# Kernel optimization log

Hardware: AMD Instinct MI355X
Metric: run time of the kernel (lower is better)

Reference implementation:

```python
import jax, jax.numpy as jnp
import numpy as np
from jax import lax


def setup_inputs() -> dict:
    key = jax.random.key(0)
    k1, k2 = jax.random.split(key)
    B, T, C, U, W = 8, 4096, 512, 512, 2
    inputs = jax.random.normal(k1, (B, T, C), dtype=jnp.float32)
    kernel = jax.random.normal(k2, (W, C, 3 * U), dtype=jnp.float32) * (1.0 / np.sqrt(W * C))
    bias = jnp.zeros((3 * U,), dtype=jnp.float32)
    return {"inputs": inputs, "kernel": kernel, "bias": bias}


def _fo_pool(x, f):
    # x, f: [B, T, U]; c_t = f_t * c_{t-1} + (1 - f_t) * x_t, c_0 = 0
    xT = jnp.swapaxes(x, 0, 1)  # [T, B, U]
    fT = jnp.swapaxes(f, 0, 1)
    c0 = jnp.zeros(x.shape[:1] + x.shape[2:], dtype=x.dtype)  # [B, U]

    def step(c, fx):
        ft, xt = fx
        c = ft * c + (1.0 - ft) * xt
        return c, c

    _, cT = lax.scan(step, c0, (fT, xT))
    return jnp.swapaxes(cT, 0, 1)  # [B, T, U]


def reference(inputs, kernel, bias):
    # Conv1D, padding='same', stride=1, NWC layout
    gates = lax.conv_general_dilated(
        inputs, kernel, window_strides=(1,), padding='SAME',
        dimension_numbers=('NWC', 'WIO', 'NWC')) + bias  # [B, T, 3U]
    x, forget, output = jnp.split(gates, 3, axis=-1)
    x = jnp.tanh(x)
    forget = jax.nn.sigmoid(forget)
    c = _fo_pool(x, forget)
    h = jax.nn.sigmoid(output) * c
    return h
```

## Files before the change

### kernel.cpp

```cpp
#include <hip/hip_runtime.h>

typedef unsigned short u16;
typedef unsigned int u32;
typedef _Float16 f16;
typedef __attribute__((ext_vector_type(8))) _Float16 half8;
typedef __attribute__((ext_vector_type(2))) __fp16 fp16x2;
typedef __attribute__((ext_vector_type(4))) float float4_;
typedef __attribute__((ext_vector_type(4))) unsigned short ushort4_;
typedef __attribute__((ext_vector_type(4))) unsigned int u32x4;

union hu { f16 h; u16 u; };

__device__ __forceinline__ u32 pkrtz(float a, float b) {
    fp16x2 t = __builtin_amdgcn_cvt_pkrtz(a, b);
    union { fp16x2 h; u32 u; } cv; cv.h = t;
    return cv.u;
}

__device__ __forceinline__ void gl16(const u16* g, u16* l) {
    __builtin_amdgcn_global_load_lds(
        (const __attribute__((address_space(1))) void*)g,
        (__attribute__((address_space(3))) void*)l, 16, 0, 0);
}

#define Bsz 8
#define Tsz 4096
#define Csz 512
#define Usz 512
#define NG  1536
#define KK  1024
#define MM  32768
#define NCH 64
#define CHL 64

__global__ void prep_a(const float* __restrict__ in, u16* __restrict__ A16) {
    int gid = blockIdx.x * 256 + threadIdx.x;
    int idx8 = gid * 8;
    int c8 = idx8 & 511;
    int row = idx8 >> 9;
    int b = (u32)row / 4097u;
    int t = row - b * 4097;
    u32x4 w;
    if (t == Tsz) {
        w = (u32x4)0;
    } else {
        const float* p = in + ((size_t)(b * Tsz + t) << 9) + c8;
        float4_ v0 = *(const float4_*)p;
        float4_ v1 = *(const float4_*)(p + 4);
        w.x = pkrtz(v0.x, v0.y); w.y = pkrtz(v0.z, v0.w);
        w.z = pkrtz(v1.x, v1.y); w.w = pkrtz(v1.z, v1.w);
    }
    *(u32x4*)(A16 + idx8) = w;
}

__global__ void prep_k(const float* __restrict__ kern, u16* __restrict__ KT) {
    int n = blockIdx.x * 256 + threadIdx.x;
    int k = blockIdx.y;
    float v = kern[(size_t)k * NG + n];
    hu cv; cv.h = (f16)v;
    KT[(size_t)n * KK + k] = cv.u;
}

__global__ __launch_bounds__(256, 4) void gemm_gates(
    const u16* __restrict__ A16, const u16* __restrict__ KT,
    const float* __restrict__ bias,
    u16* __restrict__ X, u16* __restrict__ F, float* __restrict__ O)
{
    __shared__ u16 lA[8192], lB[8192];

    const int tid  = threadIdx.x;
    const int lane = tid & 63;
    const int wave = tid >> 6;

    const int g   = blockIdx.x;
    const int grp = g / 192;
    const int r   = g - grp * 192;
    const int nb  = r % 12;
    const int mb  = grp * 16 + r / 12;
    const int m0 = mb * 128;
    const int n0 = nb * 128;
    const int b  = m0 >> 12;
    const int t0 = m0 & 4095;
    const int arow0 = b * (Tsz + 1) + t0;

    float4_ acc[4][4];
    #pragma unroll
    for (int i = 0; i < 4; ++i)
        #pragma unroll
        for (int j = 0; j < 4; ++j) acc[i][j] = (float4_)0.0f;

    const int wm = (wave >> 1) * 64;
    const int wn = (wave & 1) * 64;
    const int ar = wm + (lane & 15);
    const int br = wn + (lane & 15);
    const int q  = lane >> 4;
    const int swz = lane & 7;

    for (int kc = 0; kc < KK; kc += 64) {
        __syncthreads();
        const int tap = kc >> 9;
        const int kin = kc & 511;
        const int ab = arow0 + tap;
        #pragma unroll
        for (int it = 0; it < 4; ++it) {
            const int s = it * 256 + tid;
            const int row = s >> 3, p = s & 7;
            const int c = p ^ (row & 7);
            gl16(A16 + (((size_t)(ab + row)) << 9) + kin + c * 8, lA + (s - lane) * 8);
        }
        #pragma unroll
        for (int it = 0; it < 4; ++it) {
            const int s = it * 256 + tid;
            const int row = s >> 3, p = s & 7;
            const int c = p ^ (row & 7);
            gl16(KT + (((size_t)(n0 + row)) << 10) + kc + c * 8, lB + (s - lane) * 8);
        }
        __syncthreads();

        #pragma unroll
        for (int s2 = 0; s2 < 2; ++s2) {
            half8 fa[4], fb[4];
            const int cc = (s2 * 4 + q) ^ swz;
            #pragma unroll
            for (int i = 0; i < 4; ++i) {
                fa[i] = *(const half8*)(lA + (ar + i * 16) * 64 + cc * 8);
                fb[i] = *(const half8*)(lB + (br + i * 16) * 64 + cc * 8);
            }
            #pragma unroll
            for (int mi = 0; mi < 4; ++mi)
                #pragma unroll
                for (int ni = 0; ni < 4; ++ni)
                    acc[mi][ni] = __builtin_amdgcn_mfma_f32_16x16x32_f16(fa[mi], fb[ni], acc[mi][ni], 0, 0, 0);
        }
    }

    const int plane = nb >> 2;
    const int rq = q * 4;
    const int cl = lane & 15;
    #pragma unroll
    for (int mi = 0; mi < 4; ++mi)
        #pragma unroll
        for (int ni = 0; ni < 4; ++ni) {
            const int gm = m0 + wm + mi * 16 + rq;
            const int gn = n0 + wn + ni * 16 + cl;
            const float bv = bias[gn];
            const int cp = gn & 511;
            #pragma unroll
            for (int r2 = 0; r2 < 4; ++r2) {
                float v = acc[mi][ni][r2] + bv;
                if (plane == 0) {
                    float res = 1.0f - 2.0f / (__expf(2.0f * v) + 1.0f);
                    hu cv; cv.h = (f16)res;
                    X[(size_t)(gm + r2) * Usz + cp] = cv.u;
                } else if (plane == 1) {
                    float res = 1.0f / (1.0f + __expf(-v));
                    hu cv; cv.h = (f16)res;
                    F[(size_t)(gm + r2) * Usz + cp] = cv.u;
                } else {
                    float res = 1.0f / (1.0f + __expf(-v));
                    O[(size_t)(gm + r2) * Usz + cp] = res;
                }
            }
        }
}

__device__ __forceinline__ float4_ x4(const u16* p) {
    ushort4_ xr = *(const ushort4_*)p;
    float4_ xv;
    #pragma unroll
    for (int j = 0; j < 4; ++j) { hu cv; cv.u = xr[j]; xv[j] = (float)cv.h; }
    return xv;
}

__global__ void scan_chunk(const u16* __restrict__ F, const u16* __restrict__ X,
                           float* __restrict__ CA, float* __restrict__ CB) {
    int g = blockIdx.x * 256 + threadIdx.x;
    int u4 = (g & 127) * 4;
    int bc = g >> 7;
    size_t base = (size_t)bc * CHL * Usz + u4;
    float4_ c = (float4_)0.0f, A = (float4_)1.0f;
    for (int i = 0; i < CHL; ++i) {
        float4_ fv = x4(F + base + (size_t)i * Usz);
        float4_ xv = x4(X + base + (size_t)i * Usz);
        c = fv * c + (1.0f - fv) * xv;
        A = A * fv;
    }
    *(float4_*)(CA + (size_t)bc * Usz + u4) = A;
    *(float4_*)(CB + (size_t)bc * Usz + u4) = c;
}

__global__ void scan_prefix(const float* __restrict__ CA, const float* __restrict__ CB,
                            float* __restrict__ CS) {
    int g = blockIdx.x * 256 + threadIdx.x;
    int u = g & 511;
    int b = g >> 9;
    float c = 0.0f;
    #pragma unroll 16
    for (int ch = 0; ch < NCH; ++ch) {
        int idx = (b * NCH + ch) * Usz + u;
        CS[idx] = c;
        c = CA[idx] * c + CB[idx];
    }
}

__global__ void scan_final(const u16* __restrict__ F, const u16* __restrict__ X,
                           const float* __restrict__ CS, float* __restrict__ out) {
    int g = blockIdx.x * 256 + threadIdx.x;
    int u4 = (g & 127) * 4;
    int bc = g >> 7;
    size_t base = (size_t)bc * CHL * Usz + u4;
    float4_ c = *(const float4_*)(CS + (size_t)bc * Usz + u4);
    for (int i = 0; i < CHL; ++i) {
        float4_ fv = x4(F + base + (size_t)i * Usz);
        float4_ xv = x4(X + base + (size_t)i * Usz);
        c = fv * c + (1.0f - fv) * xv;
        float4_ ov = *(const float4_*)(out + base + (size_t)i * Usz);
        *(float4_*)(out + base + (size_t)i * Usz) = ov * c;
    }
}

extern "C" void kernel_launch(void* const* d_in, const int* in_sizes, int n_in,
                              void* d_out, int out_size, void* d_ws, size_t ws_size,
                              hipStream_t stream) {
    const float* in   = (const float*)d_in[0];
    const float* kern = (const float*)d_in[1];
    const float* bias = (const float*)d_in[2];
    float* out = (float*)d_out;
    char* ws = (char*)d_ws;

    const size_t A16_B  = (size_t)Bsz * (Tsz + 1) * Csz * 2;
    const size_t OFF_KT = A16_B;
    const size_t OFF_F  = OFF_KT + (size_t)NG * KK * 2;
    const size_t OFF_X  = OFF_F + (size_t)MM * Usz * 2;
    const size_t OFF_CA = OFF_X + (size_t)MM * Usz * 2;
    const size_t CH_B   = (size_t)Bsz * NCH * Usz * 4;
    const size_t NEED   = OFF_CA + 3 * CH_B;

    if (ws_size < NEED) return;

    u16*   A16 = (u16*)ws;
    u16*   KT  = (u16*)(ws + OFF_KT);
    u16*   Fh  = (u16*)(ws + OFF_F);
    u16*   Xb  = (u16*)(ws + OFF_X);
    float* CA  = (float*)(ws + OFF_CA);
    float* CB  = CA + CH_B / 4;
    float* CS  = CB + CH_B / 4;

    prep_a<<<(int)(A16_B / 16 / 256), 256, 0, stream>>>(in, A16);
    prep_k<<<dim3(NG / 256, KK), 256, 0, stream>>>(kern, KT);
    gemm_gates<<<(MM / 128) * (NG / 128), 256, 0, stream>>>(A16, KT, bias, Xb, Fh, out);
    scan_chunk<<<Bsz * NCH * Usz / 4 / 256, 256, 0, stream>>>(Fh, Xb, CA, CB);
    scan_prefix<<<Bsz * Usz / 256, 256, 0, stream>>>(CA, CB, CS);
    scan_final<<<Bsz * NCH * Usz / 4 / 256, 256, 0, stream>>>(Fh, Xb, CS, out);
}
```

Measured before the change: 323.1 us.

## Merge prep kernels, store output gate as fp16, retile GEMM block order

Folds the two input-conversion kernels into one launch to remove a launch boundary. When the workspace is large enough, the sigmoid output gate is stored as fp16 in scratch instead of fp32 in the output buffer, which halves that gate's write and read traffic in the GEMM epilogue and final scan. The GEMM block-to-tile mapping changes to groups of 8 M-tiles across all 12 N-tiles, and the per-iteration address computation is hoisted out of the K loop. The fp16 output gate adds rounding error, and the fast path depends on the workspace size the harness supplies.

```diff
diff --git a/kernel.cpp b/kernel.cpp
--- a/kernel.cpp
+++ b/kernel.cpp
@@ -33,38 +33,44 @@
 #define NCH 64
 #define CHL 64
 
-__global__ void prep_a(const float* __restrict__ in, u16* __restrict__ A16) {
-    int gid = blockIdx.x * 256 + threadIdx.x;
-    int idx8 = gid * 8;
-    int c8 = idx8 & 511;
-    int row = idx8 >> 9;
-    int b = (u32)row / 4097u;
-    int t = row - b * 4097;
-    u32x4 w;
-    if (t == Tsz) {
-        w = (u32x4)0;
+#define PA_BLKS 8194
+#define PK_BLKS 6144
+
+__global__ void prep(const float* __restrict__ in, u16* __restrict__ A16,
+                     const float* __restrict__ kern, u16* __restrict__ KT) {
+    if (blockIdx.x < PA_BLKS) {
+        int gid = blockIdx.x * 256 + threadIdx.x;
+        int idx8 = gid * 8;
+        int c8 = idx8 & 511;
+        int row = idx8 >> 9;
+        int b = (u32)row / 4097u;
+        int t = row - b * 4097;
+        u32x4 w;
+        if (t == Tsz) {
+            w = (u32x4)0;
+        } else {
+            const float* p = in + ((size_t)(b * Tsz + t) << 9) + c8;
+            float4_ v0 = *(const float4_*)p;
+            float4_ v1 = *(const float4_*)(p + 4);
+            w.x = pkrtz(v0.x, v0.y); w.y = pkrtz(v0.z, v0.w);
+            w.z = pkrtz(v1.x, v1.y); w.w = pkrtz(v1.z, v1.w);
+        }
+        *(u32x4*)(A16 + idx8) = w;
     } else {
-        const float* p = in + ((size_t)(b * Tsz + t) << 9) + c8;
-        float4_ v0 = *(const float4_*)p;
-        float4_ v1 = *(const float4_*)(p + 4);
-        w.x = pkrtz(v0.x, v0.y); w.y = pkrtz(v0.z, v0.w);
-        w.z = pkrtz(v1.x, v1.y); w.w = pkrtz(v1.z, v1.w);
-    }
-    *(u32x4*)(A16 + idx8) = w;
-}
-
-__global__ void prep_k(const float* __restrict__ kern, u16* __restrict__ KT) {
-    int n = blockIdx.x * 256 + threadIdx.x;
-    int k = blockIdx.y;
-    float v = kern[(size_t)k * NG + n];
-    hu cv; cv.h = (f16)v;
-    KT[(size_t)n * KK + k] = cv.u;
+        int bk = blockIdx.x - PA_BLKS;
+        int k = bk / 6;
+        int n = (bk % 6) * 256 + threadIdx.x;
+        float v = kern[(size_t)k * NG + n];
+        hu cv; cv.h = (f16)v;
+        KT[(size_t)n * KK + k] = cv.u;
+    }
 }
 
 __global__ __launch_bounds__(256, 4) void gemm_gates(
     const u16* __restrict__ A16, const u16* __restrict__ KT,
     const float* __restrict__ bias,
-    u16* __restrict__ X, u16* __restrict__ F, float* __restrict__ O)
+    u16* __restrict__ X, u16* __restrict__ F, u16* __restrict__ Oh,
+    float* __restrict__ Of, int useOh)
 {
     __shared__ u16 lA[8192], lB[8192];
 
@@ -72,11 +78,12 @@
     const int lane = tid & 63;
     const int wave = tid >> 6;
 
-    const int g   = blockIdx.x;
-    const int grp = g / 192;
-    const int r   = g - grp * 192;
-    const int nb  = r % 12;
-    const int mb  = grp * 16 + r / 12;
+    const int g    = blockIdx.x;
+    const int grp  = g / 96;
+    const int r    = g - grp * 96;
+    const int mloc = r & 7;
+    const int nb   = r >> 3;
+    const int mb   = grp * 8 + mloc;
     const int m0 = mb * 128;
     const int n0 = nb * 128;
     const int b  = m0 >> 12;
@@ -96,25 +103,27 @@
     const int q  = lane >> 4;
     const int swz = lane & 7;
 
-    for (int kc = 0; kc < KK; kc += 64) {
+    u32 aOff[4], bOff[4];
+    int ldsOff[4];
+    #pragma unroll
+    for (int it = 0; it < 4; ++it) {
+        const int s = it * 256 + tid;
+        const int row = s >> 3, p = s & 7;
+        const int c = p ^ (row & 7);
+        aOff[it] = ((u32)(arow0 + row) << 9) + c * 8;
+        bOff[it] = ((u32)(n0 + row) << 10) + c * 8;
+        ldsOff[it] = (s - lane) * 8;
+    }
+
+    #pragma unroll 4
+    for (int kk = 0; kk < KK; kk += 64) {
         __syncthreads();
-        const int tap = kc >> 9;
-        const int kin = kc & 511;
-        const int ab = arow0 + tap;
-        #pragma unroll
-        for (int it = 0; it < 4; ++it) {
-            const int s = it * 256 + tid;
-            const int row = s >> 3, p = s & 7;
-            const int c = p ^ (row & 7);
-            gl16(A16 + (((size_t)(ab + row)) << 9) + kin + c * 8, lA + (s - lane) * 8);
-        }
-        #pragma unroll
-        for (int it = 0; it < 4; ++it) {
-            const int s = it * 256 + tid;
-            const int row = s >> 3, p = s & 7;
-            const int c = p ^ (row & 7);
-            gl16(KT + (((size_t)(n0 + row)) << 10) + kc + c * 8, lB + (s - lane) * 8);
-        }
+        #pragma unroll
+        for (int it = 0; it < 4; ++it)
+            gl16(A16 + aOff[it] + kk, lA + ldsOff[it]);
+        #pragma unroll
+        for (int it = 0; it < 4; ++it)
+            gl16(KT + bOff[it] + kk, lB + ldsOff[it]);
         __syncthreads();
 
         #pragma unroll
@@ -148,17 +157,16 @@
             #pragma unroll
             for (int r2 = 0; r2 < 4; ++r2) {
                 float v = acc[mi][ni][r2] + bv;
+                const size_t idx = (size_t)(gm + r2) * Usz + cp;
                 if (plane == 0) {
                     float res = 1.0f - 2.0f / (__expf(2.0f * v) + 1.0f);
                     hu cv; cv.h = (f16)res;
-                    X[(size_t)(gm + r2) * Usz + cp] = cv.u;
-                } else if (plane == 1) {
-                    float res = 1.0f / (1.0f + __expf(-v));
-                    hu cv; cv.h = (f16)res;
-                    F[(size_t)(gm + r2) * Usz + cp] = cv.u;
+                    X[idx] = cv.u;
                 } else {
                     float res = 1.0f / (1.0f + __expf(-v));
-                    O[(size_t)(gm + r2) * Usz + cp] = res;
+                    if (plane == 1)      { hu cv; cv.h = (f16)res; F[idx] = cv.u; }
+                    else if (useOh)      { hu cv; cv.h = (f16)res; Oh[idx] = cv.u; }
+                    else                 { Of[idx] = res; }
                 }
             }
         }
@@ -203,8 +211,10 @@
     }
 }
 
+template <bool OH>
 __global__ void scan_final(const u16* __restrict__ F, const u16* __restrict__ X,
-                           const float* __restrict__ CS, float* __restrict__ out) {
+                           const u16* __restrict__ Oh, const float* __restrict__ CS,
+                           float* __restrict__ out) {
     int g = blockIdx.x * 256 + threadIdx.x;
     int u4 = (g & 127) * 4;
     int bc = g >> 7;
@@ -214,7 +224,8 @@
         float4_ fv = x4(F + base + (size_t)i * Usz);
         float4_ xv = x4(X + base + (size_t)i * Usz);
         c = fv * c + (1.0f - fv) * xv;
-        float4_ ov = *(const float4_*)(out + base + (size_t)i * Usz);
+        float4_ ov = OH ? x4(Oh + base + (size_t)i * Usz)
+                        : *(const float4_*)(out + base + (size_t)i * Usz);
         *(float4_*)(out + base + (size_t)i * Usz) = ov * c;
     }
 }
@@ -232,24 +243,30 @@
     const size_t OFF_KT = A16_B;
     const size_t OFF_F  = OFF_KT + (size_t)NG * KK * 2;
     const size_t OFF_X  = OFF_F + (size_t)MM * Usz * 2;
-    const size_t OFF_CA = OFF_X + (size_t)MM * Usz * 2;
+    const size_t OFF_O  = OFF_X + (size_t)MM * Usz * 2;
     const size_t CH_B   = (size_t)Bsz * NCH * Usz * 4;
-    const size_t NEED   = OFF_CA + 3 * CH_B;
-
-    if (ws_size < NEED) return;
+    const size_t NEED_A = OFF_O + 3 * CH_B;
+    const size_t NEED_B = OFF_O + (size_t)MM * Usz * 2 + 3 * CH_B;
+
+    if (ws_size < NEED_A) return;
+    const int useOh = ws_size >= NEED_B;
 
     u16*   A16 = (u16*)ws;
     u16*   KT  = (u16*)(ws + OFF_KT);
     u16*   Fh  = (u16*)(ws + OFF_F);
     u16*   Xb  = (u16*)(ws + OFF_X);
-    float* CA  = (float*)(ws + OFF_CA);
+    u16*   Ohp = (u16*)(ws + OFF_O);
+    const size_t caOff = useOh ? OFF_O + (size_t)MM * Usz * 2 : OFF_O;
+    float* CA  = (float*)(ws + caOff);
     float* CB  = CA + CH_B / 4;
     float* CS  = CB + CH_B / 4;
 
-    prep_a<<<(int)(A16_B / 16 / 256), 256, 0, stream>>>(in, A16);
-    prep_k<<<dim3(NG / 256, KK), 256, 0, stream>>>(kern, KT);
-    gemm_gates<<<(MM / 128) * (NG / 128), 256, 0, stream>>>(A16, KT, bias, Xb, Fh, out);
+    prep<<<PA_BLKS + PK_BLKS, 256, 0, stream>>>(in, A16, kern, KT);
+    gemm_gates<<<(MM / 128) * (NG / 128), 256, 0, stream>>>(A16, KT, bias, Xb, Fh, Ohp, out, useOh);
     scan_chunk<<<Bsz * NCH * Usz / 4 / 256, 256, 0, stream>>>(Fh, Xb, CA, CB);
     scan_prefix<<<Bsz * Usz / 256, 256, 0, stream>>>(CA, CB, CS);
-    scan_final<<<Bsz * NCH * Usz / 4 / 256, 256, 0, stream>>>(Fh, Xb, CS, out);
-}
+    if (useOh)
+        scan_final<true><<<Bsz * NCH * Usz / 4 / 256, 256, 0, stream>>>(Fh, Xb, Ohp, CS, out);
+    else
+        scan_final<false><<<Bsz * NCH * Usz / 4 / 256, 256, 0, stream>>>(Fh, Xb, Ohp, CS, out);
+}
```

After: 363.1 us. +12.4%, slower.
